# Optimization experiments

Measured on AMD Instinct MI355X. Metric: run time of the kernel, lower is better.

## Reference

```python
import jax, jax.numpy as jnp
import numpy as np

B, S, C, H = 2, 2048, 1024, 16
D = C // H  # depth per head = 64


def mish(x):
    return x * jnp.tanh(jax.nn.softplus(x))


def setup_inputs() -> dict:
    key = jax.random.key(0)
    ks = jax.random.split(key, 11)
    s = 1.0 / np.sqrt(C)
    return {
        "x": jax.random.normal(ks[0], (B, S, C), jnp.float32),
        "y": jax.random.normal(ks[1], (B, S, C), jnp.float32),
        "t_mat": jax.random.normal(ks[2], (B, S, S), jnp.float32),
        "wq": jax.random.normal(ks[3], (C, C), jnp.float32) * s,
        "bq": jnp.zeros((C,), jnp.float32),
        "wk": jax.random.normal(ks[4], (C, C), jnp.float32) * s,
        "bk": jnp.zeros((C,), jnp.float32),
        "wv": jax.random.normal(ks[5], (C, C), jnp.float32) * s,
        "bv": jnp.zeros((C,), jnp.float32),
        "wc": jax.random.normal(ks[6], (H,), jnp.float32),   # 1x1 Conv2D, 1 in-channel -> H out-channels
        "bc": jnp.zeros((H,), jnp.float32),
        "wf": jax.random.normal(ks[7], (C, C), jnp.float32) * s,  # 1x1 Conv1D == per-position Dense
        "bf": jnp.zeros((C,), jnp.float32),
    }


def _split_heads(t):
    # (B, S, C) -> (B*H, S, D)
    return t.reshape(B, S, H, D).transpose(0, 2, 1, 3).reshape(B * H, S, D)


def reference(x, y, t_mat, wq, bq, wk, bk, wv, bv, wc, bc, wf, bf):
    q = _split_heads(y @ wq + bq)   # (BH, S, D)
    k = _split_heads(x @ wk + bk)
    v = _split_heads(y @ wv + bv)

    # context: 1x1 conv + tanh over t_mat -> (B, S, S, H) -> (B*H, S, S)
    c = jnp.tanh(t_mat[..., None] * wc + bc)
    c = c.transpose(0, 3, 1, 2).reshape(B * H, S, S)

    qk = jnp.einsum("bkd,bqd->bkq", k, q) / jnp.sqrt(jnp.float32(D))  # (BH, Sk, Sq)
    cv = jnp.einsum("bks,bsd->bkd", c, v)                             # (BH, S, D)
    att = jnp.einsum("bkq,bqd->bkd", qk, cv)                          # (BH, S, D)

    # merge heads: (BH, S, D) -> (B, S, C)
    merged = att.reshape(B, H, S, D).transpose(0, 2, 1, 3).reshape(B, S, C)
    return mish(merged @ wf + bf)
```

## Files before the change

kernel.cpp:

```cpp
#include <hip/hip_runtime.h>
#include <math.h>

#define B_ 2
#define S_ 2048
#define C_ 1024
#define H_ 16
#define D_ 64

typedef __bf16 bf16_t;
typedef __attribute__((ext_vector_type(8))) __bf16 bf16x8;
typedef __attribute__((ext_vector_type(4))) __bf16 bf16x4;
typedef __attribute__((ext_vector_type(4))) float f32x4;

__device__ __forceinline__ void gload16(const void* g, void* l) {
    __builtin_amdgcn_global_load_lds(
        (const __attribute__((address_space(1))) unsigned int*)g,
        (__attribute__((address_space(3))) unsigned int*)l, 16, 0, 0);
}

__device__ __forceinline__ float tanh_fast(float z) {
    z = fminf(fmaxf(z, -12.f), 12.f);
    float e = __expf(2.f * z);
    return 1.f - __fdividef(2.f, e + 1.f);
}

__device__ __forceinline__ float mish_f(float x) {
    float sp = (x > 15.f) ? x : log1pf(__expf(x));
    return x * tanh_fast(sp);
}

__device__ __forceinline__ float tanh_folded(float t, float w2, float b2) {
    float e = __builtin_amdgcn_exp2f(fmaf(t, w2, b2));
    float r = __builtin_amdgcn_rcpf(e + 1.f);
    return fmaf(-2.f, r, 1.f);
}

__global__ __launch_bounds__(256) void cvt2_bf16(
    const float* __restrict__ a, bf16_t* __restrict__ oa,
    const float* __restrict__ b, bf16_t* __restrict__ ob)
{
    size_t i = ((size_t)blockIdx.x * 256 + threadIdx.x) * 8;
    const float* in = blockIdx.y ? b : a;
    bf16_t* out = blockIdx.y ? ob : oa;
    float4 u = *(const float4*)&in[i];
    float4 v = *(const float4*)&in[i + 4];
    bf16x8 o;
    o[0] = (bf16_t)u.x; o[1] = (bf16_t)u.y; o[2] = (bf16_t)u.z; o[3] = (bf16_t)u.w;
    o[4] = (bf16_t)v.x; o[5] = (bf16_t)v.y; o[6] = (bf16_t)v.z; o[7] = (bf16_t)v.w;
    *(bf16x8*)&out[i] = o;
}

__global__ __launch_bounds__(256) void wtrans_bf16(
    const float* __restrict__ w0, const float* __restrict__ w1,
    const float* __restrict__ w2,
    bf16_t* __restrict__ o0, bf16_t* __restrict__ o1, bf16_t* __restrict__ o2)
{
    const float* in = blockIdx.z == 0 ? w0 : (blockIdx.z == 1 ? w1 : w2);
    bf16_t* out = blockIdx.z == 0 ? o0 : (blockIdx.z == 1 ? o1 : o2);
    __shared__ float ts[64][65];
    const int t = threadIdx.x;
    const int k0 = blockIdx.y * 64, n0 = blockIdx.x * 64;
    const int r = t >> 2, c0 = (t & 3) * 16;
    #pragma unroll
    for (int j = 0; j < 16; j += 4) {
        float4 v = *(const float4*)&in[(size_t)(k0 + r) * C_ + n0 + c0 + j];
        ts[c0 + j + 0][r] = v.x; ts[c0 + j + 1][r] = v.y;
        ts[c0 + j + 2][r] = v.z; ts[c0 + j + 3][r] = v.w;
    }
    __syncthreads();
    #pragma unroll
    for (int g = 0; g < 2; ++g) {
        bf16x8 o;
        #pragma unroll
        for (int e = 0; e < 8; ++e) o[e] = (bf16_t)ts[r][c0 + g * 8 + e];
        *(bf16x8*)&out[(size_t)(n0 + r) * C_ + k0 + c0 + g * 8] = o;
    }
}

__global__ __launch_bounds__(256) void qkv_proj(
    const bf16_t* __restrict__ ybf, const bf16_t* __restrict__ xbf,
    const bf16_t* __restrict__ wqt, const bf16_t* __restrict__ wkt,
    const bf16_t* __restrict__ wvt,
    const float* __restrict__ bq, const float* __restrict__ bk,
    const float* __restrict__ bv,
    bf16_t* __restrict__ Qt, bf16_t* __restrict__ Kb, bf16_t* __restrict__ Vt)
{
    const int z = blockIdx.z;
    const bf16_t* A  = (z == 1) ? xbf : ybf;
    const bf16_t* Bt = (z == 0) ? wqt : (z == 1) ? wkt : wvt;
    const float* bias = (z == 0) ? bq : (z == 1) ? bk : bv;
    const int K = C_;

    __shared__ bf16_t As[128 * 32];
    __shared__ bf16_t Bs[128 * 32];

    const int t = threadIdx.x;
    const int w = t >> 6, lane = t & 63;
    const int wm = (w >> 1) * 64, wn = (w & 1) * 64;
    const int l15 = lane & 15, l4 = lane >> 4;
    const int row0 = blockIdx.y * 128, col0 = blockIdx.x * 128;

    const int sr = t >> 2, sk = (t & 3) * 8;
    const bf16_t* gA = A + (size_t)(row0 + sr) * K + sk;
    const bf16_t* gB = Bt + (size_t)(col0 + sr) * K + sk;
    bf16_t* lA = As + (t & ~63) * 8;
    bf16_t* lB = Bs + (t & ~63) * 8;

    f32x4 acc[4][4] = {};

    for (int k0 = 0; k0 < K; k0 += 32) {
        __syncthreads();
        gload16(gA + k0, lA);
        gload16(gA + k0 + (size_t)64 * K, lA + 2048);
        gload16(gB + k0, lB);
        gload16(gB + k0 + (size_t)64 * K, lB + 2048);
        __syncthreads();
        bf16x8 a[4], b[4];
        #pragma unroll
        for (int i = 0; i < 4; ++i)
            a[i] = *(const bf16x8*)&As[(wm + i * 16 + l15) * 32 + l4 * 8];
        #pragma unroll
        for (int j = 0; j < 4; ++j)
            b[j] = *(const bf16x8*)&Bs[(wn + j * 16 + l15) * 32 + l4 * 8];
        #pragma unroll
        for (int i = 0; i < 4; ++i)
            #pragma unroll
            for (int j = 0; j < 4; ++j)
                acc[i][j] = __builtin_amdgcn_mfma_f32_16x16x32_bf16(
                    a[i], b[j], acc[i][j], 0, 0, 0);
    }

    if (z != 1) {
        bf16_t* To = (z == 0) ? Qt : Vt;
        #pragma unroll
        for (int i = 0; i < 4; ++i) {
            int mb = row0 + wm + i * 16 + l4 * 4;
            int b2 = mb >> 11, s = mb & 2047;
            #pragma unroll
            for (int j = 0; j < 4; ++j) {
                int c = col0 + wn + j * 16 + l15;
                float bv2 = bias[c];
                bf16x4 o;
                #pragma unroll
                for (int r = 0; r < 4; ++r) o[r] = (bf16_t)(acc[i][j][r] + bv2);
                *(bf16x4*)&To[((size_t)b2 * C_ + c) * S_ + s] = o;
            }
        }
    } else {
        #pragma unroll
        for (int i = 0; i < 4; ++i)
            #pragma unroll
            for (int j = 0; j < 4; ++j) {
                int c = col0 + wn + j * 16 + l15;
                float bv2 = bias[c];
                #pragma unroll
                for (int r = 0; r < 4; ++r) {
                    int m = row0 + wm + i * 16 + l4 * 4 + r;
                    Kb[(size_t)m * C_ + c] = (bf16_t)(acc[i][j][r] + bv2);
                }
            }
    }
}

__global__ __launch_bounds__(256) void cv_mfma(
    const float* __restrict__ t_mat, const bf16_t* __restrict__ Vt,
    const float* __restrict__ wc, const float* __restrict__ bc,
    bf16_t* __restrict__ CVpt)
{
    const int bh = blockIdx.z, b = bh >> 4, h = bh & 15;
    const int q0 = blockIdx.x * 128;
    const int p = blockIdx.y;
    const int t = threadIdx.x;
    const int w = t >> 6, lane = t & 63;
    const int l15 = lane & 15, l4 = lane >> 4;

    __shared__ bf16_t As[128 * 32];
    __shared__ bf16_t Bs[64 * 32];

    const float LOG2E2 = 2.8853900817779268f;
    const float wch2 = wc[h] * LOG2E2, bch2 = bc[h] * LOG2E2;
    const float* tb = t_mat + (size_t)b * S_ * S_ + (size_t)q0 * S_;
    const bf16_t* Vb = Vt + ((size_t)b * C_ + h * 64) * S_;

    const int rr = t >> 1, sp = (t & 1) * 16;
    const int vd = t >> 2, vse = (t & 3) * 8;
    bf16_t* lB = Bs + (t & ~63) * 8;

    f32x4 acc[2][4] = {};

    const int s_beg = p * 512, s_end = s_beg + 512;
    for (int s0 = s_beg; s0 < s_end; s0 += 32) {
        const float* trow = tb + (size_t)rr * S_ + s0 + sp;
        float4 v0 = *(const float4*)&trow[0];
        float4 v1 = *(const float4*)&trow[4];
        float4 v2 = *(const float4*)&trow[8];
        float4 v3 = *(const float4*)&trow[12];
        bf16x8 p0, p1;
        p0[0] = (bf16_t)tanh_folded(v0.x, wch2, bch2);
        p0[1] = (bf16_t)tanh_folded(v0.y, wch2, bch2);
        p0[2] = (bf16_t)tanh_folded(v0.z, wch2, bch2);
        p0[3] = (bf16_t)tanh_folded(v0.w, wch2, bch2);
        p0[4] = (bf16_t)tanh_folded(v1.x, wch2, bch2);
        p0[5] = (bf16_t)tanh_folded(v1.y, wch2, bch2);
        p0[6] = (bf16_t)tanh_folded(v1.z, wch2, bch2);
        p0[7] = (bf16_t)tanh_folded(v1.w, wch2, bch2);
        p1[0] = (bf16_t)tanh_folded(v2.x, wch2, bch2);
        p1[1] = (bf16_t)tanh_folded(v2.y, wch2, bch2);
        p1[2] = (bf16_t)tanh_folded(v2.z, wch2, bch2);
        p1[3] = (bf16_t)tanh_folded(v2.w, wch2, bch2);
        p1[4] = (bf16_t)tanh_folded(v3.x, wch2, bch2);
        p1[5] = (bf16_t)tanh_folded(v3.y, wch2, bch2);
        p1[6] = (bf16_t)tanh_folded(v3.z, wch2, bch2);
        p1[7] = (bf16_t)tanh_folded(v3.w, wch2, bch2);
        __syncthreads();
        gload16(Vb + (size_t)vd * S_ + s0 + vse, lB);
        *(bf16x8*)&As[rr * 32 + sp] = p0;
        *(bf16x8*)&As[rr * 32 + sp + 8] = p1;
        __syncthreads();
        bf16x8 a0 = *(const bf16x8*)&As[(w * 32 + l15) * 32 + l4 * 8];
        bf16x8 a1 = *(const bf16x8*)&As[(w * 32 + 16 + l15) * 32 + l4 * 8];
        #pragma unroll
        for (int j = 0; j < 4; ++j) {
            bf16x8 bb = *(const bf16x8*)&Bs[(j * 16 + l15) * 32 + l4 * 8];
            acc[0][j] = __builtin_amdgcn_mfma_f32_16x16x32_bf16(a0, bb, acc[0][j], 0, 0, 0);
            acc[1][j] = __builtin_amdgcn_mfma_f32_16x16x32_bf16(a1, bb, acc[1][j], 0, 0, 0);
        }
    }

    bf16_t* outp = CVpt + ((size_t)(p * 32 + bh) * 64) * S_;
    #pragma unroll
    for (int i = 0; i < 2; ++i) {
        int q = q0 + w * 32 + i * 16 + l4 * 4;
        #pragma unroll
        for (int j = 0; j < 4; ++j) {
            int d = j * 16 + l15;
            bf16x4 o;
            #pragma unroll
            for (int r = 0; r < 4; ++r) o[r] = (bf16_t)acc[i][j][r];
            *(bf16x4*)&outp[(size_t)d * S_ + q] = o;
        }
    }
}

__global__ __launch_bounds__(256) void qtcv_mfma(
    const bf16_t* __restrict__ Qt, const bf16_t* __restrict__ CVpt,
    float* __restrict__ Mm)
{
    const int bh = blockIdx.y, b = bh >> 4, h = bh & 15;
    const int q0 = blockIdx.x * 128;
    const int t = threadIdx.x;
    const int w = t >> 6, lane = t & 63;
    const int wm = (w >> 1) * 32, wn = (w & 1) * 32;
    const int l15 = lane & 15, l4 = lane >> 4;

    __shared__ bf16_t As[64 * 32];
    __shared__ bf16_t Bs[64 * 32];

    const bf16_t* Aq = Qt + ((size_t)b * C_ + h * 64) * S_;

    const int sr = t >> 2, sk = (t & 3) * 8;
    bf16_t* lA = As + (t & ~63) * 8;
    bf16_t* lB = Bs + (t & ~63) * 8;

    f32x4 acc[2][2] = {};

    for (int qc = 0; qc < 128; qc += 32) {
        const int q = q0 + qc;
        __syncthreads();
        gload16(Aq + (size_t)sr * S_ + q + sk, lA);
        #pragma unroll
        for (int p = 0; p < 4; ++p) {
            const bf16_t* Bq = CVpt + ((size_t)(p * 32 + bh) * 64) * S_;
            __syncthreads();
            gload16(Bq + (size_t)sr * S_ + q + sk, lB);
            __syncthreads();
            bf16x8 a0 = *(const bf16x8*)&As[(wm + l15) * 32 + l4 * 8];
            bf16x8 a1 = *(const bf16x8*)&As[(wm + 16 + l15) * 32 + l4 * 8];
            bf16x8 b0 = *(const bf16x8*)&Bs[(wn + l15) * 32 + l4 * 8];
            bf16x8 b1 = *(const bf16x8*)&Bs[(wn + 16 + l15) * 32 + l4 * 8];
            acc[0][0] = __builtin_amdgcn_mfma_f32_16x16x32_bf16(a0, b0, acc[0][0], 0, 0, 0);
            acc[0][1] = __builtin_amdgcn_mfma_f32_16x16x32_bf16(a0, b1, acc[0][1], 0, 0, 0);
            acc[1][0] = __builtin_amdgcn_mfma_f32_16x16x32_bf16(a1, b0, acc[1][0], 0, 0, 0);
            acc[1][1] = __builtin_amdgcn_mfma_f32_16x16x32_bf16(a1, b1, acc[1][1], 0, 0, 0);
        }
    }

    float* mp = Mm + (size_t)bh * 64 * 64;
    #pragma unroll
    for (int i = 0; i < 2; ++i)
        #pragma unroll
        for (int j = 0; j < 2; ++j)
            #pragma unroll
            for (int r = 0; r < 4; ++r)
                atomicAdd(&mp[(size_t)(wm + i * 16 + l4 * 4 + r) * 64 +
                              wn + j * 16 + l15], acc[i][j][r]);
}

__global__ __launch_bounds__(256) void weff_kernel(
    const float* __restrict__ Mm, const float* __restrict__ wf,
    bf16_t* __restrict__ Wefft)
{
    const int b = blockIdx.z, h = blockIdx.y;
    const int co0 = blockIdx.x * 64;
    const int t = threadIdx.x;
    const int tx = t & 15, ty = t >> 4;

    __shared__ float Ms[64][64];
    __shared__ float Ws[64][64];

    const float* Mb = Mm + (size_t)(b * H_ + h) * 64 * 64;

    const int r  = t >> 2;
    const int c4 = (t & 3) << 2;

    #pragma unroll
    for (int rep = 0; rep < 4; ++rep) {
        int col = c4 + rep * 16;
        float4 m4 = *(const float4*)&Mb[(size_t)r * 64 + col];
        Ms[col + 0][r] = m4.x; Ms[col + 1][r] = m4.y;
        Ms[col + 2][r] = m4.z; Ms[col + 3][r] = m4.w;
        float4 w4 = *(const float4*)&wf[(size_t)(h * 64 + r) * C_ + co0 + col];
        *(float4*)&Ws[r][col] = w4;
    }
    __syncthreads();

    float acc[4][4] = {};
    #pragma unroll
    for (int kk = 0; kk < 64; ++kk) {
        float av[4], bv2[4];
        *(float4*)&av[0] = *(const float4*)&Ms[kk][ty * 4];
        *(float4*)&bv2[0] = *(const float4*)&Ws[kk][tx * 4];
        #pragma unroll
        for (int i = 0; i < 4; ++i)
            #pragma unroll
            for (int j = 0; j < 4; ++j)
                acc[i][j] = fmaf(av[i], bv2[j], acc[i][j]);
    }

    bf16_t* wp = Wefft + (size_t)b * C_ * C_;
    #pragma unroll
    for (int i = 0; i < 4; ++i)
        #pragma unroll
        for (int j = 0; j < 4; ++j)
            wp[(size_t)(co0 + tx * 4 + j) * C_ + h * 64 + ty * 4 + i] =
                (bf16_t)(acc[i][j] * 0.125f);
}

__global__ __launch_bounds__(256) void final_gemm(
    const bf16_t* __restrict__ Kb, const bf16_t* __restrict__ Weft,
    const float* __restrict__ bias, float* __restrict__ out)
{
    const int z = blockIdx.z;
    const bf16_t* A  = Kb + (size_t)z * S_ * C_;
    const bf16_t* Bt = Weft + (size_t)z * C_ * C_;
    float* Co = out + (size_t)z * S_ * C_;
    const int K = C_;

    __shared__ bf16_t As[128 * 32];
    __shared__ bf16_t Bs[128 * 32];

    const int t = threadIdx.x;
    const int w = t >> 6, lane = t & 63;
    const int wm = (w >> 1) * 64, wn = (w & 1) * 64;
    const int l15 = lane & 15, l4 = lane >> 4;
    const int row0 = blockIdx.y * 128, col0 = blockIdx.x * 128;

    const int sr = t >> 2, sk = (t & 3) * 8;
    const bf16_t* gA = A + (size_t)(row0 + sr) * K + sk;
    const bf16_t* gB = Bt + (size_t)(col0 + sr) * K + sk;
    bf16_t* lA = As + (t & ~63) * 8;
    bf16_t* lB = Bs + (t & ~63) * 8;

    f32x4 acc[4][4] = {};

    for (int k0 = 0; k0 < K; k0 += 32) {
        __syncthreads();
        gload16(gA + k0, lA);
        gload16(gA + k0 + (size_t)64 * K, lA + 2048);
        gload16(gB + k0, lB);
        gload16(gB + k0 + (size_t)64 * K, lB + 2048);
        __syncthreads();
        bf16x8 a[4], b[4];
        #pragma unroll
        for (int i = 0; i < 4; ++i)
            a[i] = *(const bf16x8*)&As[(wm + i * 16 + l15) * 32 + l4 * 8];
        #pragma unroll
        for (int j = 0; j < 4; ++j)
            b[j] = *(const bf16x8*)&Bs[(wn + j * 16 + l15) * 32 + l4 * 8];
        #pragma unroll
        for (int i = 0; i < 4; ++i)
            #pragma unroll
            for (int j = 0; j < 4; ++j)
                acc[i][j] = __builtin_amdgcn_mfma_f32_16x16x32_bf16(
                    a[i], b[j], acc[i][j], 0, 0, 0);
    }

    #pragma unroll
    for (int i = 0; i < 4; ++i)
        #pragma unroll
        for (int j = 0; j < 4; ++j) {
            int c = col0 + wn + j * 16 + l15;
            float bv2 = bias[c];
            #pragma unroll
            for (int r = 0; r < 4; ++r) {
                int m = row0 + wm + i * 16 + l4 * 4 + r;
                Co[(size_t)m * C_ + c] = mish_f(acc[i][j][r] + bv2);
            }
        }
}

extern "C" void kernel_launch(void* const* d_in, const int* in_sizes, int n_in,
                              void* d_out, int out_size, void* d_ws, size_t ws_size,
                              hipStream_t stream) {
    const float* x     = (const float*)d_in[0];
    const float* y     = (const float*)d_in[1];
    const float* t_mat = (const float*)d_in[2];
    const float* wq    = (const float*)d_in[3];
    const float* bq    = (const float*)d_in[4];
    const float* wk    = (const float*)d_in[5];
    const float* bk    = (const float*)d_in[6];
    const float* wv    = (const float*)d_in[7];
    const float* bv    = (const float*)d_in[8];
    const float* wc    = (const float*)d_in[9];
    const float* bc    = (const float*)d_in[10];
    const float* wf    = (const float*)d_in[11];
    const float* bf    = (const float*)d_in[12];
    float* out = (float*)d_out;

    char* base = (char*)d_ws;
    bf16_t* Qt   = (bf16_t*)(base + 0);
    bf16_t* Kb   = (bf16_t*)(base + 8388608);
    bf16_t* Vt   = (bf16_t*)(base + 16777216);
    float*  Mm   = (float*) (base + 25165824);
    bf16_t* Weft = (bf16_t*)(base + 25690112);
    bf16_t* ybf  = (bf16_t*)(base + 29884416);
    bf16_t* xbf  = (bf16_t*)(base + 38273024);
    bf16_t* wqt  = (bf16_t*)(base + 46661632);
    bf16_t* wkt  = (bf16_t*)(base + 48758784);
    bf16_t* wvt  = (bf16_t*)(base + 50855936);
    bf16_t* CVpt = (bf16_t*)(base + 29884416);

    hipMemsetAsync(Mm, 0, (size_t)B_ * H_ * 64 * 64 * sizeof(float), stream);

    dim3 blk(256);

    cvt2_bf16<<<dim3((B_ * S_ * C_) / (256 * 8), 2), blk, 0, stream>>>(
        y, ybf, x, xbf);
    wtrans_bf16<<<dim3(16, 16, 3), blk, 0, stream>>>(wq, wk, wv, wqt, wkt, wvt);

    qkv_proj<<<dim3(C_ / 128, (B_ * S_) / 128, 3), blk, 0, stream>>>(
        ybf, xbf, wqt, wkt, wvt, bq, bk, bv, Qt, Kb, Vt);

    cv_mfma<<<dim3(S_ / 128, 4, B_ * H_), blk, 0, stream>>>(
        t_mat, Vt, wc, bc, CVpt);

    qtcv_mfma<<<dim3(16, B_ * H_), blk, 0, stream>>>(Qt, CVpt, Mm);

    weff_kernel<<<dim3(C_ / 64, H_, B_), blk, 0, stream>>>(Mm, wf, Weft);

    final_gemm<<<dim3(C_ / 128, S_ / 128, B_), blk, 0, stream>>>(
        Kb, Weft, bf, out);
}
```

Measured before the change: 295.3 us.

## Fuse context-value and Q^T·CV reduction into one kernel; shrink final GEMM tile

The cv and qtcv kernels are merged into one. Each block now stages its partial CV tile in shared memory and immediately multiplies it by the matching Q slice, accumulating into Mm with atomics. This removes the bf16 CVpt round trip through global memory and one kernel launch, at the cost of many more atomic adds into Mm. Separately, the final GEMM tile goes from 128x128 to 128x64, doubling the number of blocks to raise occupancy while lowering data reuse per block.

```diff
diff --git a/kernel.cpp b/kernel.cpp
--- a/kernel.cpp
+++ b/kernel.cpp
@@ -162,10 +162,11 @@
     }
 }
 
-__global__ __launch_bounds__(256) void cv_mfma(
+__global__ __launch_bounds__(256) void cv_qtcv_fused(
     const float* __restrict__ t_mat, const bf16_t* __restrict__ Vt,
+    const bf16_t* __restrict__ Qt,
     const float* __restrict__ wc, const float* __restrict__ bc,
-    bf16_t* __restrict__ CVpt)
+    float* __restrict__ Mm)
 {
     const int bh = blockIdx.z, b = bh >> 4, h = bh & 15;
     const int q0 = blockIdx.x * 128;
@@ -174,8 +175,10 @@
     const int w = t >> 6, lane = t & 63;
     const int l15 = lane & 15, l4 = lane >> 4;
 
-    __shared__ bf16_t As[128 * 32];
-    __shared__ bf16_t Bs[64 * 32];
+    __shared__ bf16_t smem[10240];
+    bf16_t* As = smem;
+    bf16_t* Bs = smem + 4096;
+    bf16_t* cvs = smem;
 
     const float LOG2E2 = 2.8853900817779268f;
     const float wch2 = wc[h] * LOG2E2, bch2 = bc[h] * LOG2E2;
@@ -227,73 +230,38 @@
         }
     }
 
-    bf16_t* outp = CVpt + ((size_t)(p * 32 + bh) * 64) * S_;
-    #pragma unroll
-    for (int i = 0; i < 2; ++i) {
-        int q = q0 + w * 32 + i * 16 + l4 * 4;
+    __syncthreads();
+    #pragma unroll
+    for (int i = 0; i < 2; ++i)
         #pragma unroll
         for (int j = 0; j < 4; ++j) {
             int d = j * 16 + l15;
             bf16x4 o;
             #pragma unroll
             for (int r = 0; r < 4; ++r) o[r] = (bf16_t)acc[i][j][r];
-            *(bf16x4*)&outp[(size_t)d * S_ + q] = o;
-        }
-    }
-}
-
-__global__ __launch_bounds__(256) void qtcv_mfma(
-    const bf16_t* __restrict__ Qt, const bf16_t* __restrict__ CVpt,
-    float* __restrict__ Mm)
-{
-    const int bh = blockIdx.y, b = bh >> 4, h = bh & 15;
-    const int q0 = blockIdx.x * 128;
-    const int t = threadIdx.x;
-    const int w = t >> 6, lane = t & 63;
-    const int wm = (w >> 1) * 32, wn = (w & 1) * 32;
-    const int l15 = lane & 15, l4 = lane >> 4;
-
-    __shared__ bf16_t As[64 * 32];
-    __shared__ bf16_t Bs[64 * 32];
-
-    const bf16_t* Aq = Qt + ((size_t)b * C_ + h * 64) * S_;
-
-    const int sr = t >> 2, sk = (t & 3) * 8;
-    bf16_t* lA = As + (t & ~63) * 8;
-    bf16_t* lB = Bs + (t & ~63) * 8;
-
-    f32x4 acc[2][2] = {};
-
-    for (int qc = 0; qc < 128; qc += 32) {
-        const int q = q0 + qc;
-        __syncthreads();
-        gload16(Aq + (size_t)sr * S_ + q + sk, lA);
-        #pragma unroll
-        for (int p = 0; p < 4; ++p) {
-            const bf16_t* Bq = CVpt + ((size_t)(p * 32 + bh) * 64) * S_;
-            __syncthreads();
-            gload16(Bq + (size_t)sr * S_ + q + sk, lB);
-            __syncthreads();
-            bf16x8 a0 = *(const bf16x8*)&As[(wm + l15) * 32 + l4 * 8];
-            bf16x8 a1 = *(const bf16x8*)&As[(wm + 16 + l15) * 32 + l4 * 8];
-            bf16x8 b0 = *(const bf16x8*)&Bs[(wn + l15) * 32 + l4 * 8];
-            bf16x8 b1 = *(const bf16x8*)&Bs[(wn + 16 + l15) * 32 + l4 * 8];
-            acc[0][0] = __builtin_amdgcn_mfma_f32_16x16x32_bf16(a0, b0, acc[0][0], 0, 0, 0);
-            acc[0][1] = __builtin_amdgcn_mfma_f32_16x16x32_bf16(a0, b1, acc[0][1], 0, 0, 0);
-            acc[1][0] = __builtin_amdgcn_mfma_f32_16x16x32_bf16(a1, b0, acc[1][0], 0, 0, 0);
-            acc[1][1] = __builtin_amdgcn_mfma_f32_16x16x32_bf16(a1, b1, acc[1][1], 0, 0, 0);
+            *(bf16x4*)&cvs[(size_t)w * 2560 + d * 40 + i * 16 + l4 * 4] = o;
+        }
+    __syncthreads();
+
+    const bf16_t* Qrow = Qt + ((size_t)b * C_ + h * 64 + w * 16 + l15) * S_ + q0 + l4 * 8;
+    f32x4 macc[4] = {};
+    #pragma unroll
+    for (int c = 0; c < 4; ++c) {
+        bf16x8 a = *(const bf16x8*)&Qrow[c * 32];
+        #pragma unroll
+        for (int j = 0; j < 4; ++j) {
+            bf16x8 bb = *(const bf16x8*)&cvs[(size_t)c * 2560 + (j * 16 + l15) * 40 + l4 * 8];
+            macc[j] = __builtin_amdgcn_mfma_f32_16x16x32_bf16(a, bb, macc[j], 0, 0, 0);
         }
     }
 
     float* mp = Mm + (size_t)bh * 64 * 64;
     #pragma unroll
-    for (int i = 0; i < 2; ++i)
-        #pragma unroll
-        for (int j = 0; j < 2; ++j)
-            #pragma unroll
-            for (int r = 0; r < 4; ++r)
-                atomicAdd(&mp[(size_t)(wm + i * 16 + l4 * 4 + r) * 64 +
-                              wn + j * 16 + l15], acc[i][j][r]);
+    for (int j = 0; j < 4; ++j)
+        #pragma unroll
+        for (int r = 0; r < 4; ++r)
+            atomicAdd(&mp[(size_t)(w * 16 + l4 * 4 + r) * 64 + j * 16 + l15],
+                      macc[j][r]);
 }
 
 __global__ __launch_bounds__(256) void weff_kernel(
@@ -357,13 +325,12 @@
     const int K = C_;
 
     __shared__ bf16_t As[128 * 32];
-    __shared__ bf16_t Bs[128 * 32];
+    __shared__ bf16_t Bs[64 * 32];
 
     const int t = threadIdx.x;
     const int w = t >> 6, lane = t & 63;
-    const int wm = (w >> 1) * 64, wn = (w & 1) * 64;
     const int l15 = lane & 15, l4 = lane >> 4;
-    const int row0 = blockIdx.y * 128, col0 = blockIdx.x * 128;
+    const int row0 = blockIdx.y * 128, col0 = blockIdx.x * 64;
 
     const int sr = t >> 2, sk = (t & 3) * 8;
     const bf16_t* gA = A + (size_t)(row0 + sr) * K + sk;
@@ -371,39 +338,33 @@
     bf16_t* lA = As + (t & ~63) * 8;
     bf16_t* lB = Bs + (t & ~63) * 8;
 
-    f32x4 acc[4][4] = {};
+    f32x4 acc[2][4] = {};
 
     for (int k0 = 0; k0 < K; k0 += 32) {
         __syncthreads();
         gload16(gA + k0, lA);
         gload16(gA + k0 + (size_t)64 * K, lA + 2048);
         gload16(gB + k0, lB);
-        gload16(gB + k0 + (size_t)64 * K, lB + 2048);
-        __syncthreads();
-        bf16x8 a[4], b[4];
-        #pragma unroll
-        for (int i = 0; i < 4; ++i)
-            a[i] = *(const bf16x8*)&As[(wm + i * 16 + l15) * 32 + l4 * 8];
-        #pragma unroll
-        for (int j = 0; j < 4; ++j)
-            b[j] = *(const bf16x8*)&Bs[(wn + j * 16 + l15) * 32 + l4 * 8];
-        #pragma unroll
-        for (int i = 0; i < 4; ++i)
-            #pragma unroll
-            for (int j = 0; j < 4; ++j)
-                acc[i][j] = __builtin_amdgcn_mfma_f32_16x16x32_bf16(
-                    a[i], b[j], acc[i][j], 0, 0, 0);
-    }
-
-    #pragma unroll
-    for (int i = 0; i < 4; ++i)
+        __syncthreads();
+        bf16x8 a0 = *(const bf16x8*)&As[(w * 32 + l15) * 32 + l4 * 8];
+        bf16x8 a1 = *(const bf16x8*)&As[(w * 32 + 16 + l15) * 32 + l4 * 8];
         #pragma unroll
         for (int j = 0; j < 4; ++j) {
-            int c = col0 + wn + j * 16 + l15;
+            bf16x8 bb = *(const bf16x8*)&Bs[(j * 16 + l15) * 32 + l4 * 8];
+            acc[0][j] = __builtin_amdgcn_mfma_f32_16x16x32_bf16(a0, bb, acc[0][j], 0, 0, 0);
+            acc[1][j] = __builtin_amdgcn_mfma_f32_16x16x32_bf16(a1, bb, acc[1][j], 0, 0, 0);
+        }
+    }
+
+    #pragma unroll
+    for (int i = 0; i < 2; ++i)
+        #pragma unroll
+        for (int j = 0; j < 4; ++j) {
+            int c = col0 + j * 16 + l15;
             float bv2 = bias[c];
             #pragma unroll
             for (int r = 0; r < 4; ++r) {
-                int m = row0 + wm + i * 16 + l4 * 4 + r;
+                int m = row0 + w * 32 + i * 16 + l4 * 4 + r;
                 Co[(size_t)m * C_ + c] = mish_f(acc[i][j][r] + bv2);
             }
         }
@@ -438,7 +399,6 @@
     bf16_t* wqt  = (bf16_t*)(base + 46661632);
     bf16_t* wkt  = (bf16_t*)(base + 48758784);
     bf16_t* wvt  = (bf16_t*)(base + 50855936);
-    bf16_t* CVpt = (bf16_t*)(base + 29884416);
 
     hipMemsetAsync(Mm, 0, (size_t)B_ * H_ * 64 * 64 * sizeof(float), stream);
 
@@ -451,13 +411,11 @@
     qkv_proj<<<dim3(C_ / 128, (B_ * S_) / 128, 3), blk, 0, stream>>>(
         ybf, xbf, wqt, wkt, wvt, bq, bk, bv, Qt, Kb, Vt);
 
-    cv_mfma<<<dim3(S_ / 128, 4, B_ * H_), blk, 0, stream>>>(
-        t_mat, Vt, wc, bc, CVpt);
-
-    qtcv_mfma<<<dim3(16, B_ * H_), blk, 0, stream>>>(Qt, CVpt, Mm);
+    cv_qtcv_fused<<<dim3(S_ / 128, 4, B_ * H_), blk, 0, stream>>>(
+        t_mat, Vt, Qt, wc, bc, Mm);
 
     weff_kernel<<<dim3(C_ / 64, H_, B_), blk, 0, stream>>>(Mm, wf, Weft);
 
-    final_gemm<<<dim3(C_ / 128, S_ / 128, B_), blk, 0, stream>>>(
+    final_gemm<<<dim3(C_ / 64, S_ / 128, B_), blk, 0, stream>>>(
         Kb, Weft, bf, out);
 }
```

After: 277.3 us. 6.1% less time.
